# Performance work log

Measured on AMD Instinct MI355X. Metric: run time of the kernel, lower is better.

The kernel has to match this reference:

```python
import jax, jax.numpy as jnp
import numpy as np

N = 100000
D_IN = 256
C = 4          # num_classes
D_C = 32       # output_dim // num_classes
E = 1600000    # nnz per class adjacency


def setup_inputs() -> dict:
    key = jax.random.key(0)
    k1, k2, k3, k4, k5 = jax.random.split(key, 5)
    x = jax.random.normal(k1, (N, D_IN), dtype=jnp.float32)
    # kernel (input_dim, output_dim) split along axis=1 into C chunks -> [D_IN, C, D_C]
    W = jax.random.normal(k2, (D_IN, C, D_C), dtype=jnp.float32) * (2.0 / D_IN) ** 0.5
    rows = jax.random.randint(k3, (C, E), 0, N, dtype=jnp.int64)
    cols = jax.random.randint(k4, (C, E), 0, N, dtype=jnp.int64)
    vals = jax.random.uniform(k5, (C, E), dtype=jnp.float32)
    return {"x": x, "W": W, "rows": rows, "cols": cols, "vals": vals}


def reference(x, W, rows, cols, vals):
    # dropout with rate 0.0 is identity.
    n = x.shape[0]
    # per-class dense transform: tmp[:, c, :] = x @ W[:, c, :]
    tmp = jnp.einsum('nd,dcf->ncf', x, W)  # [N, C, D_C]

    def prop(r, c, v, t):
        # t: [N, D_C] features for one class; SpMM A_c @ t via gather+segment_sum
        msg = t[c] * v[:, None]                              # [E, D_C]
        return jax.ops.segment_sum(msg, r, num_segments=n)   # [N, D_C]

    out = jax.vmap(prop, in_axes=(0, 0, 0, 1))(rows, cols, vals, tmp)  # [C, N, D_C]
    z = jnp.transpose(out, (1, 0, 2)).reshape(n, -1)  # concat along feature axis -> [N, C*D_C]
    return jax.nn.relu(z)
```

## Files before the change

kernel.cpp:

```cpp
#include <hip/hip_runtime.h>
#include <hip/hip_bf16.h>
#include <hip/hip_fp16.h>

#define D_IN 256
#define D_OUT 128
#define D_C 32
#define NUM_C 4
#define RB_LOG 10
#define RB 1024
#define MB_MAX 400

typedef _Float16 f16x8 __attribute__((ext_vector_type(8)));
typedef float    f32x4 __attribute__((ext_vector_type(4)));

__global__ void wcvt_kernel(const float* __restrict__ W, __half* __restrict__ Wt) {
    int t = blockIdx.x * 256 + threadIdx.x;
    if (t >= D_IN * D_OUT) return;
    int col = t >> 8;
    int k   = t & 255;
    Wt[col * D_IN + k] = __float2half(W[k * D_OUT + col]);
}

__global__ __launch_bounds__(256) void gemm_hist_kernel(const float* __restrict__ x,
                                                        const __half* __restrict__ Wt,
                                                        __half* __restrict__ tmp,
                                                        int Nrows,
                                                        const int* __restrict__ rows,
                                                        int* __restrict__ bcnt,
                                                        int CE, int E, int NB, int MB,
                                                        int gemmBlocks) {
    __shared__ f16x8 As[2048];
    __shared__ int   h[MB_MAX];
    const int t = threadIdx.x;

    if (blockIdx.x < gemmBlocks) {
        const int brow = blockIdx.x * 64;
        const int w   = t >> 6;
        const int l   = t & 63;
        const int l15 = l & 15;
        const int hi  = l >> 4;

        f16x8 bf[8][2];
        #pragma unroll
        for (int ks = 0; ks < 8; ++ks)
            #pragma unroll
            for (int cti = 0; cti < 2; ++cti)
                bf[ks][cti] = *reinterpret_cast<const f16x8*>(
                    Wt + (size_t)((w * 2 + cti) * 16 + l15) * D_IN + ks * 32 + hi * 8);

        #pragma unroll
        for (int i = 0; i < 8; ++i) {
            int ci  = i * 256 + t;
            int row = ci >> 5;
            int kc  = ci & 31;
            int grow = brow + row;
            float4 a0 = make_float4(0.f, 0.f, 0.f, 0.f);
            float4 a1 = make_float4(0.f, 0.f, 0.f, 0.f);
            if (grow < Nrows) {
                const float* src = x + (size_t)grow * D_IN + kc * 8;
                a0 = *reinterpret_cast<const float4*>(src);
                a1 = *reinterpret_cast<const float4*>(src + 4);
            }
            f16x8 hh;
            hh[0] = (_Float16)a0.x; hh[1] = (_Float16)a0.y;
            hh[2] = (_Float16)a0.z; hh[3] = (_Float16)a0.w;
            hh[4] = (_Float16)a1.x; hh[5] = (_Float16)a1.y;
            hh[6] = (_Float16)a1.z; hh[7] = (_Float16)a1.w;
            As[kc * 64 + (row ^ kc)] = hh;
        }
        __syncthreads();

        f32x4 acc[4][2] = {};
        #pragma unroll
        for (int rt = 0; rt < 4; ++rt) {
            const int arow = rt * 16 + l15;
            #pragma unroll
            for (int ks = 0; ks < 8; ++ks) {
                const int kcA = ks * 4 + hi;
                f16x8 afrag = As[kcA * 64 + (arow ^ kcA)];
                acc[rt][0] = __builtin_amdgcn_mfma_f32_16x16x32_f16(afrag, bf[ks][0], acc[rt][0], 0, 0, 0);
                acc[rt][1] = __builtin_amdgcn_mfma_f32_16x16x32_f16(afrag, bf[ks][1], acc[rt][1], 0, 0, 0);
            }
        }

        #pragma unroll
        for (int rt = 0; rt < 4; ++rt)
            #pragma unroll
            for (int cti = 0; cti < 2; ++cti) {
                const int cio = cti * 16 + l15;
                #pragma unroll
                for (int r = 0; r < 4; ++r) {
                    int grow = brow + rt * 16 + hi * 4 + r;
                    if (grow < Nrows)
                        tmp[((size_t)w * Nrows + grow) * 32 + cio] = __float2half((float)acc[rt][cti][r]);
                }
            }
    } else {
        const int bid = blockIdx.x - gemmBlocks;
        for (int i = t; i < MB; i += 256) h[i] = 0;
        __syncthreads();
        const int CE4 = CE >> 2;
        const int4* rows4 = reinterpret_cast<const int4*>(rows);
        int base4 = bid * 4096;
        #pragma unroll 4
        for (int i = 0; i < 16; ++i) {
            int i4 = base4 + t + i * 256;
            if (i4 < CE4) {
                int e0 = i4 << 2;
                int c = (e0 >= 3 * E) ? 3 : (e0 >= 2 * E) ? 2 : (e0 >= E) ? 1 : 0;
                int4 rv = rows4[i4];
                atomicAdd(&h[c * NB + (rv.x >> RB_LOG)], 1);
                atomicAdd(&h[c * NB + (rv.y >> RB_LOG)], 1);
                atomicAdd(&h[c * NB + (rv.z >> RB_LOG)], 1);
                atomicAdd(&h[c * NB + (rv.w >> RB_LOG)], 1);
            }
        }
        if (bid == 0 && t < (CE & 3)) {
            int e = (CE4 << 2) + t;
            int c = (e >= 3 * E) ? 3 : (e >= 2 * E) ? 2 : (e >= E) ? 1 : 0;
            atomicAdd(&h[c * NB + (rows[e] >> RB_LOG)], 1);
        }
        __syncthreads();
        for (int i = t; i < MB; i += 256)
            if (h[i]) atomicAdd(&bcnt[i], h[i]);
    }
}

__global__ __launch_bounds__(512) void bucket_scan_kernel(const int* __restrict__ bcnt,
                                                          int* __restrict__ bstartP,
                                                          int* __restrict__ bheadLine,
                                                          int* __restrict__ bstartD,
                                                          int* __restrict__ starts,
                                                          int MB, int M, int slackLines) {
    __shared__ int sd[512];
    int t = threadIdx.x;
    int v = (t < MB) ? bcnt[t] : 0;
    int capL = ((v + 7) >> 3) + slackLines;
    sd[t] = capL; __syncthreads();
    for (int off = 1; off < 512; off <<= 1) {
        int add = (t >= off) ? sd[t - off] : 0;
        __syncthreads();
        sd[t] += add;
        __syncthreads();
    }
    int exclL = sd[t] - capL;
    if (t < MB) { bstartP[t] = exclL * 8; bheadLine[t] = exclL; }
    __syncthreads();
    sd[t] = v; __syncthreads();
    for (int off = 1; off < 512; off <<= 1) {
        int add = (t >= off) ? sd[t - off] : 0;
        __syncthreads();
        sd[t] += add;
        __syncthreads();
    }
    int exclD = sd[t] - v;
    if (t < MB) bstartD[t] = exclD;
    if (t == 511) starts[M] = sd[511];
}

__global__ __launch_bounds__(512) void partition_kernel(const int* __restrict__ rows,
                                                        const int* __restrict__ cols,
                                                        const float* __restrict__ vals,
                                                        int* __restrict__ bheadLine,
                                                        int2* __restrict__ arena,
                                                        int CE, int E, int NB, int MB) {
    __shared__ int lcnt[MB_MAX];
    __shared__ int lbase[MB_MAX];
    const int t = threadIdx.x;
    for (int i = t; i < MB; i += 512) lcnt[i] = 0;
    __syncthreads();
    const int base = blockIdx.x * 8192;
    const int end  = min(base + 8192, CE);

    {
        int aStart = base;
        int nvec4 = (end - base) >> 2;
        const int4* rows4 = reinterpret_cast<const int4*>(rows + base);
        #pragma unroll 4
        for (int i = 0; i < 4; ++i) {
            int i4 = t + i * 512;
            if (i4 < nvec4) {
                int e0 = base + (i4 << 2);
                int c = (e0 >= 3 * E) ? 3 : (e0 >= 2 * E) ? 2 : (e0 >= E) ? 1 : 0;
                int4 rv = rows4[i4];
                atomicAdd(&lcnt[c * NB + (rv.x >> RB_LOG)], 1);
                atomicAdd(&lcnt[c * NB + (rv.y >> RB_LOG)], 1);
                atomicAdd(&lcnt[c * NB + (rv.z >> RB_LOG)], 1);
                atomicAdd(&lcnt[c * NB + (rv.w >> RB_LOG)], 1);
            }
        }
        int tail0 = aStart + (nvec4 << 2);
        int e = tail0 + t;
        if (e < end) {
            int c = (e >= 3 * E) ? 3 : (e >= 2 * E) ? 2 : (e >= E) ? 1 : 0;
            atomicAdd(&lcnt[c * NB + (rows[e] >> RB_LOG)], 1);
        }
    }
    __syncthreads();

    for (int b = t; b < MB; b += 512) {
        int n = lcnt[b];
        lbase[b] = n ? atomicAdd(&bheadLine[b], (n + 7) >> 3) * 8 : 0;
    }
    __syncthreads();
    for (int i = t; i < MB; i += 512) lcnt[i] = 0;
    __syncthreads();

    for (int i = 0; i < 16; ++i) {
        int e = base + t + i * 512;
        if (e < end) {
            int c = (e >= 3 * E) ? 3 : (e >= 2 * E) ? 2 : (e >= E) ? 1 : 0;
            int r = rows[e];
            int b = c * NB + (r >> RB_LOG);
            int rank = atomicAdd(&lcnt[b], 1);
            arena[lbase[b] + rank] = make_int2(cols[e] | ((r & (RB - 1)) << 17),
                                               __float_as_int(vals[e]));
        }
    }
    __syncthreads();

    for (int b = t; b < MB; b += 512) {
        int n = lcnt[b];
        if (n) {
            int endp = ((n + 7) >> 3) * 8;
            for (int s2 = n; s2 < endp; ++s2)
                arena[lbase[b] + s2] = make_int2(-1, 0);
        }
    }
}

__global__ __launch_bounds__(1024) void rowsort_kernel(const int* __restrict__ bstartP,
                                                       const int* __restrict__ bheadLine,
                                                       const int* __restrict__ bstartD,
                                                       const int2* __restrict__ src,
                                                       unsigned* __restrict__ dst,
                                                       int* __restrict__ starts,
                                                       int N, int NB) {
    __shared__ int lcnt[RB];
    __shared__ int sd[RB];
    int b = blockIdx.x;
    int c = b / NB, rb = b - c * NB;
    int t = threadIdx.x;
    int s = bstartP[b];
    int nspan = bheadLine[b] * 8 - s;
    int dbase = bstartD[b];

    lcnt[t] = 0;
    __syncthreads();
    for (int i = t; i < nspan; i += 1024) {
        unsigned u = (unsigned)src[s + i].x;
        if ((u & 0x1FFFFu) != 0x1FFFFu)
            atomicAdd(&lcnt[(u >> 17) & (RB - 1)], 1);
    }
    __syncthreads();
    int v = lcnt[t];
    sd[t] = v; __syncthreads();
    for (int off = 1; off < 1024; off <<= 1) {
        int add = (t >= off) ? sd[t - off] : 0;
        __syncthreads();
        sd[t] += add;
        __syncthreads();
    }
    int excl = sd[t] - v;
    int grow = (rb << RB_LOG) + t;
    if (grow < N) starts[c * N + grow] = dbase + excl;
    __syncthreads();
    lcnt[t] = excl;
    __syncthreads();
    for (int i = t; i < nspan; i += 1024) {
        int2 rec = src[s + i];
        unsigned u = (unsigned)rec.x;
        if ((u & 0x1FFFFu) != 0x1FFFFu) {
            int rl  = (u >> 17) & (RB - 1);
            int pos = atomicAdd(&lcnt[rl], 1);
            __half h = __float2half(__int_as_float(rec.y));
            unsigned hb = (unsigned)*reinterpret_cast<unsigned short*>(&h);
            dst[dbase + pos] = (hb << 17) | (u & 0x1FFFFu);
        }
    }
}

__global__ __launch_bounds__(256) void pull2_kernel(const int* __restrict__ starts,
                                                    const unsigned* __restrict__ arena,
                                                    const uint2* __restrict__ tmp4,
                                                    float* __restrict__ out,
                                                    int N, int M) {
    int p = blockIdx.x * 32 + (threadIdx.x >> 3);
    if (p >= M) return;
    const int lf = threadIdx.x & 7;
    int c   = p / N;
    int row = p - c * N;
    int s = starts[p];
    int n = starts[p + 1] - s;
    const uint2* tc = tmp4 + (size_t)c * N * 8 + lf;

    float4 acc = make_float4(0.f, 0.f, 0.f, 0.f);
    int base = 0;
    for (; base + 16 <= n; base += 16) {
        unsigned r[16];
        #pragma unroll
        for (int j = 0; j < 16; ++j) r[j] = arena[s + base + j];
        #pragma unroll
        for (int j = 0; j < 16; ++j) {
            unsigned short hb = (unsigned short)(r[j] >> 17);
            float v = __half2float(*reinterpret_cast<__half*>(&hb));
            uint2 tw = tc[(size_t)(r[j] & 0x1FFFFu) * 8];
            float2 t0 = __half22float2(*reinterpret_cast<__half2*>(&tw.x));
            float2 t1 = __half22float2(*reinterpret_cast<__half2*>(&tw.y));
            acc.x = fmaf(v, t0.x, acc.x);
            acc.y = fmaf(v, t0.y, acc.y);
            acc.z = fmaf(v, t1.x, acc.z);
            acc.w = fmaf(v, t1.y, acc.w);
        }
    }
    if (base + 8 <= n) {
        unsigned r[8];
        #pragma unroll
        for (int j = 0; j < 8; ++j) r[j] = arena[s + base + j];
        #pragma unroll
        for (int j = 0; j < 8; ++j) {
            unsigned short hb = (unsigned short)(r[j] >> 17);
            float v = __half2float(*reinterpret_cast<__half*>(&hb));
            uint2 tw = tc[(size_t)(r[j] & 0x1FFFFu) * 8];
            float2 t0 = __half22float2(*reinterpret_cast<__half2*>(&tw.x));
            float2 t1 = __half22float2(*reinterpret_cast<__half2*>(&tw.y));
            acc.x = fmaf(v, t0.x, acc.x);
            acc.y = fmaf(v, t0.y, acc.y);
            acc.z = fmaf(v, t1.x, acc.z);
            acc.w = fmaf(v, t1.y, acc.w);
        }
        base += 8;
    }
    for (; base < n; ++base) {
        unsigned u = arena[s + base];
        unsigned short hb = (unsigned short)(u >> 17);
        float v = __half2float(*reinterpret_cast<__half*>(&hb));
        uint2 tw = tc[(size_t)(u & 0x1FFFFu) * 8];
        float2 t0 = __half22float2(*reinterpret_cast<__half2*>(&tw.x));
        float2 t1 = __half22float2(*reinterpret_cast<__half2*>(&tw.y));
        acc.x = fmaf(v, t0.x, acc.x);
        acc.y = fmaf(v, t0.y, acc.y);
        acc.z = fmaf(v, t1.x, acc.z);
        acc.w = fmaf(v, t1.y, acc.w);
    }
    *reinterpret_cast<float4*>(&out[(size_t)row * D_OUT + c * D_C + 4 * lf]) =
        make_float4(fmaxf(acc.x, 0.f), fmaxf(acc.y, 0.f),
                    fmaxf(acc.z, 0.f), fmaxf(acc.w, 0.f));
}

__global__ __launch_bounds__(256) void scatter_kernel(const int* __restrict__ rows,
                                                      const int* __restrict__ cols,
                                                      const float* __restrict__ vals,
                                                      const __half* __restrict__ tmp,
                                                      float* __restrict__ out,
                                                      long long totalEdges, int E, int N) {
    long long gid = (long long)blockIdx.x * 8 + (threadIdx.x >> 5);
    if (gid >= totalEdges) return;
    const int lane = threadIdx.x & 31;
    const long long e1 = E, e2 = 2LL * E, e3 = 3LL * E;
    int c = (gid >= e3) ? 3 : (gid >= e2) ? 2 : (gid >= e1) ? 1 : 0;
    const float tv = __half2float(tmp[((size_t)c * N + cols[gid]) * 32 + lane]);
    atomicAdd(&out[(size_t)rows[gid] * D_OUT + c * D_C + lane], tv * vals[gid]);
}

__global__ void relu_kernel(float* __restrict__ out, int n4) {
    int i = blockIdx.x * blockDim.x + threadIdx.x;
    if (i < n4) {
        float4 v = reinterpret_cast<float4*>(out)[i];
        v.x = fmaxf(v.x, 0.f); v.y = fmaxf(v.y, 0.f);
        v.z = fmaxf(v.z, 0.f); v.w = fmaxf(v.w, 0.f);
        reinterpret_cast<float4*>(out)[i] = v;
    }
}

extern "C" void kernel_launch(void* const* d_in, const int* in_sizes, int n_in,
                              void* d_out, int out_size, void* d_ws, size_t ws_size,
                              hipStream_t stream) {
    const float* x    = (const float*)d_in[0];
    const float* W    = (const float*)d_in[1];
    const int*   rows = (const int*)d_in[2];
    const int*   cols = (const int*)d_in[3];
    const float* vals = (const float*)d_in[4];
    float* out = (float*)d_out;

    const int N  = in_sizes[0] / D_IN;
    const int CE = in_sizes[2];
    const int E  = CE / NUM_C;
    const int NB = (N + RB - 1) >> RB_LOG;
    const int MB = NUM_C * NB;
    const int M  = NUM_C * N;

    const int partBlocks = (CE + 8191) / 8192;
    const int slackLines = (7 * partBlocks + 7) / 8 + 1;
    const long long capRecs = (long long)((CE + 7) & ~7) + (long long)MB * slackLines * 8 + (long long)MB * 8;

    size_t off = 0;
    __half* tmp  = (__half*)((char*)d_ws + off); off += (size_t)N * D_OUT * 2;
    off = (off + 15) & ~(size_t)15;
    __half* Wt   = (__half*)((char*)d_ws + off); off += (size_t)D_IN * D_OUT * 2;
    int* bcnt    = (int*)((char*)d_ws + off);   off += (size_t)MB * 4;
    int* bstartP = (int*)((char*)d_ws + off);   off += (size_t)MB * 4;
    int* bheadL  = (int*)((char*)d_ws + off);   off += (size_t)MB * 4;
    int* bstartD = (int*)((char*)d_ws + off);   off += (size_t)MB * 4;
    int* starts  = (int*)((char*)d_ws + off);   off += (size_t)(M + 1) * 4;
    off = (off + 63) & ~(size_t)63;
    int2* arena  = (int2*)((char*)d_ws + off);  off += (size_t)capRecs * 8;
    unsigned* sorted = (unsigned*)((char*)d_ws + off); off += (size_t)CE * 4;
    const bool ok = (off <= ws_size) && (MB <= MB_MAX) && (MB <= 512);

    wcvt_kernel<<<(D_IN * D_OUT + 255) / 256, 256, 0, stream>>>(W, Wt);

    const int gemmBlocks = (N + 63) / 64;
    const int histBlocks = ((CE >> 2) + 4095) / 4096;
    hipMemsetAsync(bcnt, 0, (size_t)MB * 4, stream);
    gemm_hist_kernel<<<gemmBlocks + histBlocks, 256, 0, stream>>>(
        x, Wt, tmp, N, rows, bcnt, CE, E, NB, MB, gemmBlocks);

    if (ok) {
        bucket_scan_kernel<<<1, 512, 0, stream>>>(bcnt, bstartP, bheadL, bstartD, starts, MB, M, slackLines);
        partition_kernel<<<partBlocks, 512, 0, stream>>>(rows, cols, vals, bheadL, arena, CE, E, NB, MB);
        rowsort_kernel<<<MB, 1024, 0, stream>>>(bstartP, bheadL, bstartD, arena, sorted, starts, N, NB);
        const int pullBlocks = (M + 31) / 32;
        pull2_kernel<<<pullBlocks, 256, 0, stream>>>(starts, sorted,
                                                     reinterpret_cast<const uint2*>(tmp), out, N, M);
    } else {
        hipMemsetAsync(d_out, 0, (size_t)out_size * sizeof(float), stream);
        const int scatterBlocks = (CE + 7) / 8;
        scatter_kernel<<<scatterBlocks, 256, 0, stream>>>(rows, cols, vals, tmp, out, (long long)CE, E, N);
        const int n4 = out_size / 4;
        relu_kernel<<<(n4 + 255) / 256, 256, 0, stream>>>(out, n4);
    }
}
```

Baseline: 289.7 us.

## Fuse dense GEMM with partition kernel instead of histogram kernel

Moves the x@W MFMA GEMM out of the histogram launch and co-schedules it with the edge partition kernel in one grid, so the histogram runs alone and the GEMM overlaps with partitioning. GEMM blocks now use 512 threads covering 128 rows (two row-halves per class), with a 64KB shared buffer shared by both roles. The aim is better balance, since partitioning is scatter-bound and the GEMM is compute and stream-bound. In exchange the larger shared allocation and 512-thread blocks may lower occupancy for the partition blocks.

After: 274.8 us. 1.05x faster.

```diff
diff --git a/kernel.cpp b/kernel.cpp
--- a/kernel.cpp
+++ b/kernel.cpp
@@ -21,109 +21,37 @@
     Wt[col * D_IN + k] = __float2half(W[k * D_OUT + col]);
 }
 
-__global__ __launch_bounds__(256) void gemm_hist_kernel(const float* __restrict__ x,
-                                                        const __half* __restrict__ Wt,
-                                                        __half* __restrict__ tmp,
-                                                        int Nrows,
-                                                        const int* __restrict__ rows,
-                                                        int* __restrict__ bcnt,
-                                                        int CE, int E, int NB, int MB,
-                                                        int gemmBlocks) {
-    __shared__ f16x8 As[2048];
-    __shared__ int   h[MB_MAX];
+__global__ __launch_bounds__(256) void bucket_hist_kernel(const int* __restrict__ rows,
+                                                          int* __restrict__ bcnt,
+                                                          int CE, int E, int NB, int MB) {
+    __shared__ int h[MB_MAX];
     const int t = threadIdx.x;
-
-    if (blockIdx.x < gemmBlocks) {
-        const int brow = blockIdx.x * 64;
-        const int w   = t >> 6;
-        const int l   = t & 63;
-        const int l15 = l & 15;
-        const int hi  = l >> 4;
-
-        f16x8 bf[8][2];
-        #pragma unroll
-        for (int ks = 0; ks < 8; ++ks)
-            #pragma unroll
-            for (int cti = 0; cti < 2; ++cti)
-                bf[ks][cti] = *reinterpret_cast<const f16x8*>(
-                    Wt + (size_t)((w * 2 + cti) * 16 + l15) * D_IN + ks * 32 + hi * 8);
-
-        #pragma unroll
-        for (int i = 0; i < 8; ++i) {
-            int ci  = i * 256 + t;
-            int row = ci >> 5;
-            int kc  = ci & 31;
-            int grow = brow + row;
-            float4 a0 = make_float4(0.f, 0.f, 0.f, 0.f);
-            float4 a1 = make_float4(0.f, 0.f, 0.f, 0.f);
-            if (grow < Nrows) {
-                const float* src = x + (size_t)grow * D_IN + kc * 8;
-                a0 = *reinterpret_cast<const float4*>(src);
-                a1 = *reinterpret_cast<const float4*>(src + 4);
-            }
-            f16x8 hh;
-            hh[0] = (_Float16)a0.x; hh[1] = (_Float16)a0.y;
-            hh[2] = (_Float16)a0.z; hh[3] = (_Float16)a0.w;
-            hh[4] = (_Float16)a1.x; hh[5] = (_Float16)a1.y;
-            hh[6] = (_Float16)a1.z; hh[7] = (_Float16)a1.w;
-            As[kc * 64 + (row ^ kc)] = hh;
-        }
-        __syncthreads();
-
-        f32x4 acc[4][2] = {};
-        #pragma unroll
-        for (int rt = 0; rt < 4; ++rt) {
-            const int arow = rt * 16 + l15;
-            #pragma unroll
-            for (int ks = 0; ks < 8; ++ks) {
-                const int kcA = ks * 4 + hi;
-                f16x8 afrag = As[kcA * 64 + (arow ^ kcA)];
-                acc[rt][0] = __builtin_amdgcn_mfma_f32_16x16x32_f16(afrag, bf[ks][0], acc[rt][0], 0, 0, 0);
-                acc[rt][1] = __builtin_amdgcn_mfma_f32_16x16x32_f16(afrag, bf[ks][1], acc[rt][1], 0, 0, 0);
-            }
-        }
-
-        #pragma unroll
-        for (int rt = 0; rt < 4; ++rt)
-            #pragma unroll
-            for (int cti = 0; cti < 2; ++cti) {
-                const int cio = cti * 16 + l15;
-                #pragma unroll
-                for (int r = 0; r < 4; ++r) {
-                    int grow = brow + rt * 16 + hi * 4 + r;
-                    if (grow < Nrows)
-                        tmp[((size_t)w * Nrows + grow) * 32 + cio] = __float2half((float)acc[rt][cti][r]);
-                }
-            }
-    } else {
-        const int bid = blockIdx.x - gemmBlocks;
-        for (int i = t; i < MB; i += 256) h[i] = 0;
-        __syncthreads();
-        const int CE4 = CE >> 2;
-        const int4* rows4 = reinterpret_cast<const int4*>(rows);
-        int base4 = bid * 4096;
-        #pragma unroll 4
-        for (int i = 0; i < 16; ++i) {
-            int i4 = base4 + t + i * 256;
-            if (i4 < CE4) {
-                int e0 = i4 << 2;
-                int c = (e0 >= 3 * E) ? 3 : (e0 >= 2 * E) ? 2 : (e0 >= E) ? 1 : 0;
-                int4 rv = rows4[i4];
-                atomicAdd(&h[c * NB + (rv.x >> RB_LOG)], 1);
-                atomicAdd(&h[c * NB + (rv.y >> RB_LOG)], 1);
-                atomicAdd(&h[c * NB + (rv.z >> RB_LOG)], 1);
-                atomicAdd(&h[c * NB + (rv.w >> RB_LOG)], 1);
-            }
-        }
-        if (bid == 0 && t < (CE & 3)) {
-            int e = (CE4 << 2) + t;
-            int c = (e >= 3 * E) ? 3 : (e >= 2 * E) ? 2 : (e >= E) ? 1 : 0;
-            atomicAdd(&h[c * NB + (rows[e] >> RB_LOG)], 1);
-        }
-        __syncthreads();
-        for (int i = t; i < MB; i += 256)
-            if (h[i]) atomicAdd(&bcnt[i], h[i]);
-    }
+    for (int i = t; i < MB; i += 256) h[i] = 0;
+    __syncthreads();
+    const int CE4 = CE >> 2;
+    const int4* rows4 = reinterpret_cast<const int4*>(rows);
+    int base4 = blockIdx.x * 4096;
+    #pragma unroll 4
+    for (int i = 0; i < 16; ++i) {
+        int i4 = base4 + t + i * 256;
+        if (i4 < CE4) {
+            int e0 = i4 << 2;
+            int c = (e0 >= 3 * E) ? 3 : (e0 >= 2 * E) ? 2 : (e0 >= E) ? 1 : 0;
+            int4 rv = rows4[i4];
+            atomicAdd(&h[c * NB + (rv.x >> RB_LOG)], 1);
+            atomicAdd(&h[c * NB + (rv.y >> RB_LOG)], 1);
+            atomicAdd(&h[c * NB + (rv.z >> RB_LOG)], 1);
+            atomicAdd(&h[c * NB + (rv.w >> RB_LOG)], 1);
+        }
+    }
+    if (blockIdx.x == 0 && t < (CE & 3)) {
+        int e = (CE4 << 2) + t;
+        int c = (e >= 3 * E) ? 3 : (e >= 2 * E) ? 2 : (e >= E) ? 1 : 0;
+        atomicAdd(&h[c * NB + (rows[e] >> RB_LOG)], 1);
+    }
+    __syncthreads();
+    for (int i = t; i < MB; i += 256)
+        if (h[i]) atomicAdd(&bcnt[i], h[i]);
 }
 
 __global__ __launch_bounds__(512) void bucket_scan_kernel(const int* __restrict__ bcnt,
@@ -158,74 +86,146 @@
     if (t == 511) starts[M] = sd[511];
 }
 
-__global__ __launch_bounds__(512) void partition_kernel(const int* __restrict__ rows,
+__global__ __launch_bounds__(512) void part_gemm_kernel(const int* __restrict__ rows,
                                                         const int* __restrict__ cols,
                                                         const float* __restrict__ vals,
                                                         int* __restrict__ bheadLine,
                                                         int2* __restrict__ arena,
-                                                        int CE, int E, int NB, int MB) {
-    __shared__ int lcnt[MB_MAX];
-    __shared__ int lbase[MB_MAX];
+                                                        int CE, int E, int NB, int MB,
+                                                        int partBlocks,
+                                                        const float* __restrict__ x,
+                                                        const __half* __restrict__ Wt,
+                                                        __half* __restrict__ tmp,
+                                                        int Nrows) {
+    __shared__ __align__(16) char smem[65536];
     const int t = threadIdx.x;
-    for (int i = t; i < MB; i += 512) lcnt[i] = 0;
-    __syncthreads();
-    const int base = blockIdx.x * 8192;
-    const int end  = min(base + 8192, CE);
-
-    {
-        int aStart = base;
-        int nvec4 = (end - base) >> 2;
-        const int4* rows4 = reinterpret_cast<const int4*>(rows + base);
-        #pragma unroll 4
-        for (int i = 0; i < 4; ++i) {
-            int i4 = t + i * 512;
-            if (i4 < nvec4) {
-                int e0 = base + (i4 << 2);
-                int c = (e0 >= 3 * E) ? 3 : (e0 >= 2 * E) ? 2 : (e0 >= E) ? 1 : 0;
-                int4 rv = rows4[i4];
-                atomicAdd(&lcnt[c * NB + (rv.x >> RB_LOG)], 1);
-                atomicAdd(&lcnt[c * NB + (rv.y >> RB_LOG)], 1);
-                atomicAdd(&lcnt[c * NB + (rv.z >> RB_LOG)], 1);
-                atomicAdd(&lcnt[c * NB + (rv.w >> RB_LOG)], 1);
-            }
-        }
-        int tail0 = aStart + (nvec4 << 2);
-        int e = tail0 + t;
-        if (e < end) {
-            int c = (e >= 3 * E) ? 3 : (e >= 2 * E) ? 2 : (e >= E) ? 1 : 0;
-            atomicAdd(&lcnt[c * NB + (rows[e] >> RB_LOG)], 1);
-        }
-    }
-    __syncthreads();
-
-    for (int b = t; b < MB; b += 512) {
-        int n = lcnt[b];
-        lbase[b] = n ? atomicAdd(&bheadLine[b], (n + 7) >> 3) * 8 : 0;
-    }
-    __syncthreads();
-    for (int i = t; i < MB; i += 512) lcnt[i] = 0;
-    __syncthreads();
-
-    for (int i = 0; i < 16; ++i) {
-        int e = base + t + i * 512;
-        if (e < end) {
-            int c = (e >= 3 * E) ? 3 : (e >= 2 * E) ? 2 : (e >= E) ? 1 : 0;
-            int r = rows[e];
-            int b = c * NB + (r >> RB_LOG);
-            int rank = atomicAdd(&lcnt[b], 1);
-            arena[lbase[b] + rank] = make_int2(cols[e] | ((r & (RB - 1)) << 17),
-                                               __float_as_int(vals[e]));
-        }
-    }
-    __syncthreads();
-
-    for (int b = t; b < MB; b += 512) {
-        int n = lcnt[b];
-        if (n) {
-            int endp = ((n + 7) >> 3) * 8;
-            for (int s2 = n; s2 < endp; ++s2)
-                arena[lbase[b] + s2] = make_int2(-1, 0);
-        }
+
+    if (blockIdx.x < partBlocks) {
+        int* lcnt  = (int*)smem;
+        int* lbase = lcnt + MB_MAX;
+        for (int i = t; i < MB; i += 512) lcnt[i] = 0;
+        __syncthreads();
+        const int base = blockIdx.x * 8192;
+        const int end  = min(base + 8192, CE);
+
+        {
+            int nvec4 = (end - base) >> 2;
+            const int4* rows4 = reinterpret_cast<const int4*>(rows + base);
+            #pragma unroll 4
+            for (int i = 0; i < 4; ++i) {
+                int i4 = t + i * 512;
+                if (i4 < nvec4) {
+                    int e0 = base + (i4 << 2);
+                    int c = (e0 >= 3 * E) ? 3 : (e0 >= 2 * E) ? 2 : (e0 >= E) ? 1 : 0;
+                    int4 rv = rows4[i4];
+                    atomicAdd(&lcnt[c * NB + (rv.x >> RB_LOG)], 1);
+                    atomicAdd(&lcnt[c * NB + (rv.y >> RB_LOG)], 1);
+                    atomicAdd(&lcnt[c * NB + (rv.z >> RB_LOG)], 1);
+                    atomicAdd(&lcnt[c * NB + (rv.w >> RB_LOG)], 1);
+                }
+            }
+            int e = base + (nvec4 << 2) + t;
+            if (e < end) {
+                int c = (e >= 3 * E) ? 3 : (e >= 2 * E) ? 2 : (e >= E) ? 1 : 0;
+                atomicAdd(&lcnt[c * NB + (rows[e] >> RB_LOG)], 1);
+            }
+        }
+        __syncthreads();
+
+        for (int b = t; b < MB; b += 512) {
+            int n = lcnt[b];
+            lbase[b] = n ? atomicAdd(&bheadLine[b], (n + 7) >> 3) * 8 : 0;
+        }
+        __syncthreads();
+        for (int i = t; i < MB; i += 512) lcnt[i] = 0;
+        __syncthreads();
+
+        for (int i = 0; i < 16; ++i) {
+            int e = base + t + i * 512;
+            if (e < end) {
+                int c = (e >= 3 * E) ? 3 : (e >= 2 * E) ? 2 : (e >= E) ? 1 : 0;
+                int r = rows[e];
+                int b = c * NB + (r >> RB_LOG);
+                int rank = atomicAdd(&lcnt[b], 1);
+                arena[lbase[b] + rank] = make_int2(cols[e] | ((r & (RB - 1)) << 17),
+                                                   __float_as_int(vals[e]));
+            }
+        }
+        __syncthreads();
+
+        for (int b = t; b < MB; b += 512) {
+            int n = lcnt[b];
+            if (n) {
+                int endp = ((n + 7) >> 3) * 8;
+                for (int s2 = n; s2 < endp; ++s2)
+                    arena[lbase[b] + s2] = make_int2(-1, 0);
+            }
+        }
+    } else {
+        f16x8* As = (f16x8*)smem;
+        const int brow = (blockIdx.x - partBlocks) * 128;
+        const int w   = t >> 6;
+        const int cls = w & 3;
+        const int rh  = w >> 2;
+        const int l   = t & 63;
+        const int l15 = l & 15;
+        const int hi  = l >> 4;
+
+        f16x8 bf[8][2];
+        #pragma unroll
+        for (int ks = 0; ks < 8; ++ks)
+            #pragma unroll
+            for (int cti = 0; cti < 2; ++cti)
+                bf[ks][cti] = *reinterpret_cast<const f16x8*>(
+                    Wt + (size_t)((cls * 2 + cti) * 16 + l15) * D_IN + ks * 32 + hi * 8);
+
+        #pragma unroll
+        for (int i = 0; i < 8; ++i) {
+            int ci  = i * 512 + t;
+            int row = ci >> 5;
+            int kc  = ci & 31;
+            int grow = brow + row;
+            float4 a0 = make_float4(0.f, 0.f, 0.f, 0.f);
+            float4 a1 = make_float4(0.f, 0.f, 0.f, 0.f);
+            if (grow < Nrows) {
+                const float* src = x + (size_t)grow * D_IN + kc * 8;
+                a0 = *reinterpret_cast<const float4*>(src);
+                a1 = *reinterpret_cast<const float4*>(src + 4);
+            }
+            f16x8 hh;
+            hh[0] = (_Float16)a0.x; hh[1] = (_Float16)a0.y;
+            hh[2] = (_Float16)a0.z; hh[3] = (_Float16)a0.w;
+            hh[4] = (_Float16)a1.x; hh[5] = (_Float16)a1.y;
+            hh[6] = (_Float16)a1.z; hh[7] = (_Float16)a1.w;
+            As[kc * 128 + (row ^ kc)] = hh;
+        }
+        __syncthreads();
+
+        f32x4 acc[4][2] = {};
+        #pragma unroll
+        for (int rt = 0; rt < 4; ++rt) {
+            const int arow = rh * 64 + rt * 16 + l15;
+            #pragma unroll
+            for (int ks = 0; ks < 8; ++ks) {
+                const int kcA = ks * 4 + hi;
+                f16x8 afrag = As[kcA * 128 + (arow ^ kcA)];
+                acc[rt][0] = __builtin_amdgcn_mfma_f32_16x16x32_f16(afrag, bf[ks][0], acc[rt][0], 0, 0, 0);
+                acc[rt][1] = __builtin_amdgcn_mfma_f32_16x16x32_f16(afrag, bf[ks][1], acc[rt][1], 0, 0, 0);
+            }
+        }
+
+        #pragma unroll
+        for (int rt = 0; rt < 4; ++rt)
+            #pragma unroll
+            for (int cti = 0; cti < 2; ++cti) {
+                const int cio = cti * 16 + l15;
+                #pragma unroll
+                for (int r = 0; r < 4; ++r) {
+                    int grow = brow + rh * 64 + rt * 16 + hi * 4 + r;
+                    if (grow < Nrows)
+                        tmp[((size_t)cls * Nrows + grow) * 32 + cio] = __float2half((float)acc[rt][cti][r]);
+                }
+            }
     }
 }
 
@@ -391,6 +391,7 @@
     const int M  = NUM_C * N;
 
     const int partBlocks = (CE + 8191) / 8192;
+    const int gemmBlocks = (N + 127) / 128;
     const int slackLines = (7 * partBlocks + 7) / 8 + 1;
     const long long capRecs = (long long)((CE + 7) & ~7) + (long long)MB * slackLines * 8 + (long long)MB * 8;
 
@@ -410,20 +411,20 @@
 
     wcvt_kernel<<<(D_IN * D_OUT + 255) / 256, 256, 0, stream>>>(W, Wt);
 
-    const int gemmBlocks = (N + 63) / 64;
-    const int histBlocks = ((CE >> 2) + 4095) / 4096;
-    hipMemsetAsync(bcnt, 0, (size_t)MB * 4, stream);
-    gemm_hist_kernel<<<gemmBlocks + histBlocks, 256, 0, stream>>>(
-        x, Wt, tmp, N, rows, bcnt, CE, E, NB, MB, gemmBlocks);
-
     if (ok) {
+        hipMemsetAsync(bcnt, 0, (size_t)MB * 4, stream);
+        const int histBlocks = ((CE >> 2) + 4095) / 4096;
+        bucket_hist_kernel<<<histBlocks, 256, 0, stream>>>(rows, bcnt, CE, E, NB, MB);
         bucket_scan_kernel<<<1, 512, 0, stream>>>(bcnt, bstartP, bheadL, bstartD, starts, MB, M, slackLines);
-        partition_kernel<<<partBlocks, 512, 0, stream>>>(rows, cols, vals, bheadL, arena, CE, E, NB, MB);
+        part_gemm_kernel<<<partBlocks + gemmBlocks, 512, 0, stream>>>(
+            rows, cols, vals, bheadL, arena, CE, E, NB, MB, partBlocks, x, Wt, tmp, N);
         rowsort_kernel<<<MB, 1024, 0, stream>>>(bstartP, bheadL, bstartD, arena, sorted, starts, N, NB);
         const int pullBlocks = (M + 31) / 32;
         pull2_kernel<<<pullBlocks, 256, 0, stream>>>(starts, sorted,
                                                      reinterpret_cast<const uint2*>(tmp), out, N, M);
     } else {
+        part_gemm_kernel<<<gemmBlocks, 512, 0, stream>>>(
+            rows, cols, vals, bheadL, arena, CE, E, NB, MB, 0, x, Wt, tmp, N);
         hipMemsetAsync(d_out, 0, (size_t)out_size * sizeof(float), stream);
         const int scatterBlocks = (CE + 7) / 8;
         scatter_kernel<<<scatterBlocks, 256, 0, stream>>>(rows, cols, vals, tmp, out, (long long)CE, E, N);
```
